# Optimization experiments

Measured on AMD Instinct MI355X. Metric: run time of the kernel, lower is better.

The kernel has to match this reference:

```python
import jax, jax.numpy as jnp
import numpy as np

B, S, DIM = 2, 2048, 2048
N_HEADS, N_KV = 16, 4
HEAD_DIM = DIM // N_HEADS
THETA = 10000.0


def _rope_tables(seq, half, theta):
    inv_freq = 1.0 / (theta ** (jnp.arange(0, half, dtype=jnp.float32) / half))
    t = jnp.arange(seq, dtype=jnp.float32)
    freqs = jnp.outer(t, inv_freq)  # (seq, half)
    return jnp.cos(freqs), jnp.sin(freqs)


def setup_inputs() -> dict:
    key = jax.random.key(0)
    ks = jax.random.split(key, 6)
    cos, sin = _rope_tables(S, HEAD_DIM // 2, THETA)
    scale_in = 1.0 / np.sqrt(DIM)
    return {
        "x": jax.random.normal(ks[0], (B, S, DIM), dtype=jnp.float32),
        "cos": cos,
        "sin": sin,
        "attn_mask": jax.random.randint(ks[1], (B, 1, 1, S), 0, 2) > 0,
        "Wq": jax.random.normal(ks[2], (N_HEADS * HEAD_DIM, DIM), dtype=jnp.float32) * scale_in,
        "Wk": jax.random.normal(ks[3], (N_KV * HEAD_DIM, DIM), dtype=jnp.float32) * scale_in,
        "Wv": jax.random.normal(ks[4], (N_KV * HEAD_DIM, DIM), dtype=jnp.float32) * scale_in,
        "Wo": jax.random.normal(ks[5], (DIM, N_HEADS * HEAD_DIM), dtype=jnp.float32) * scale_in,
    }


def _apply_rope(x, cos, sin):
    # x: (B, H, S, D); cos/sin: (S, D//2)
    D = x.shape[-1]
    x1, x2 = x[..., : D // 2], x[..., D // 2:]
    c = cos[None, None, : x.shape[2]]
    s = sin[None, None, : x.shape[2]]
    return jnp.concatenate([x1 * c - x2 * s, x1 * s + x2 * c], axis=-1)


def reference(x, cos, sin, attn_mask, Wq, Wk, Wv, Wo):
    b, s, _ = x.shape
    d = 2 * cos.shape[1]
    h = Wq.shape[0] // d
    kvh = Wk.shape[0] // d
    g = h // kvh  # query heads per KV head

    q = (x @ Wq.T).reshape(b, s, h, d).transpose(0, 2, 1, 3)     # (B,H,S,D)
    k = (x @ Wk.T).reshape(b, s, kvh, d).transpose(0, 2, 1, 3)   # (B,KV,S,D)
    v = (x @ Wv.T).reshape(b, s, kvh, d).transpose(0, 2, 1, 3)

    q = _apply_rope(q, cos, sin)
    k = _apply_rope(k, cos, sin)

    # Grouped attention without materializing repeated KV.
    qg = q.reshape(b, kvh, g, s, d)
    scores = jnp.einsum("bkgsd,bktd->bkgst", qg, k) / jnp.sqrt(jnp.asarray(d, q.dtype))
    mask = attn_mask[:, :, None]  # (B,1,1,1,S) broadcast over (B,KV,G,S,T)
    scores = jnp.where(mask, -jnp.inf, scores)
    attn = jax.nn.softmax(scores, axis=-1)
    out = jnp.einsum("bkgst,bktd->bkgsd", attn, v)
    out = out.reshape(b, h, s, d).transpose(0, 2, 1, 3).reshape(b, s, h * d)
    return out @ Wo.T
```

## Files before the change

kernel.cpp:

```cpp
#include <hip/hip_runtime.h>

typedef __attribute__((ext_vector_type(8))) short s16x8;
typedef __attribute__((ext_vector_type(4))) float f32x4;

#define B_    2
#define S_    2048
#define DIM_  2048
#define H_    16
#define KVH_  4
#define HD_   128
#define NQKV  3072

static __device__ __forceinline__ unsigned short f2bf(float f) {
  unsigned int u = __float_as_uint(f);
  u += 0x7fff + ((u >> 16) & 1);
  return (unsigned short)(u >> 16);
}
static __device__ __forceinline__ float bf2f(unsigned short h) {
  return __uint_as_float(((unsigned int)h) << 16);
}

__global__ __launch_bounds__(256) void cast_f32_bf16(const float* __restrict__ src,
                                                     unsigned short* __restrict__ dst, int n) {
  int i = (blockIdx.x * 256 + threadIdx.x) * 8;
  if (i >= n) return;
  float4 a = *(const float4*)(src + i);
  float4 b = *(const float4*)(src + i + 4);
  uint4 o;
  o.x = (unsigned)f2bf(a.x) | ((unsigned)f2bf(a.y) << 16);
  o.y = (unsigned)f2bf(a.z) | ((unsigned)f2bf(a.w) << 16);
  o.z = (unsigned)f2bf(b.x) | ((unsigned)f2bf(b.y) << 16);
  o.w = (unsigned)f2bf(b.z) | ((unsigned)f2bf(b.w) << 16);
  *(uint4*)(dst + i) = o;
}

template <bool BF16OUT>
__global__ __launch_bounds__(256) void gemm_bt(const unsigned short* __restrict__ A,
                                               const unsigned short* __restrict__ Bw,
                                               void* __restrict__ Cp, int N, int K) {
  __shared__ __align__(16) unsigned short As[128 * 32];
  __shared__ __align__(16) unsigned short Bs[128 * 32];
  const int tid = threadIdx.x;
  const int n0 = blockIdx.x * 128, m0 = blockIdx.y * 128;
  const int w = tid >> 6, l = tid & 63;
  const int wr = w >> 1, wc = w & 1;
  const int lo = l & 15, hi = l >> 4;
  f32x4 acc[4][4] = {};
  const int KT = K >> 5;
  for (int kt = 0; kt < KT; ++kt) {
    const int k0 = kt << 5;
    __syncthreads();
#pragma unroll
    for (int c = 0; c < 2; ++c) {
      int idx = tid + c * 256;
      int row = idx >> 2, ko = (idx & 3) << 3;
      __builtin_amdgcn_global_load_lds(
          (__attribute__((address_space(1))) void*)(A + (size_t)(m0 + row) * K + k0 + ko),
          (__attribute__((address_space(3))) void*)(As + idx * 8), 16, 0, 0);
      __builtin_amdgcn_global_load_lds(
          (__attribute__((address_space(1))) void*)(Bw + (size_t)(n0 + row) * K + k0 + ko),
          (__attribute__((address_space(3))) void*)(Bs + idx * 8), 16, 0, 0);
    }
    asm volatile("s_waitcnt vmcnt(0)" ::: "memory");
    __syncthreads();
    s16x8 af[4], bfr[4];
#pragma unroll
    for (int mi = 0; mi < 4; ++mi)
      af[mi] = *(const s16x8*)(As + (wr * 64 + mi * 16 + lo) * 32 + hi * 8);
#pragma unroll
    for (int ni = 0; ni < 4; ++ni)
      bfr[ni] = *(const s16x8*)(Bs + (wc * 64 + ni * 16 + lo) * 32 + hi * 8);
#pragma unroll
    for (int mi = 0; mi < 4; ++mi)
#pragma unroll
      for (int ni = 0; ni < 4; ++ni)
        acc[mi][ni] = __builtin_amdgcn_mfma_f32_16x16x32_bf16(af[mi], bfr[ni], acc[mi][ni], 0, 0, 0);
  }
#pragma unroll
  for (int mi = 0; mi < 4; ++mi) {
#pragma unroll
    for (int ni = 0; ni < 4; ++ni) {
      int col = n0 + wc * 64 + ni * 16 + lo;
      int rowb = m0 + wr * 64 + mi * 16 + hi * 4;
#pragma unroll
      for (int r = 0; r < 4; ++r) {
        float v = acc[mi][ni][r];
        if (BF16OUT)
          ((unsigned short*)Cp)[(size_t)(rowb + r) * N + col] = f2bf(v);
        else
          ((float*)Cp)[(size_t)(rowb + r) * N + col] = v;
      }
    }
  }
}

__global__ __launch_bounds__(256) void rope_kernel(const unsigned short* __restrict__ QKV,
                                                   const float* __restrict__ ctab,
                                                   const float* __restrict__ stab,
                                                   unsigned short* __restrict__ dst,
                                                   int nheads, int coloff, float scale) {
  int gid = blockIdx.x * 256 + threadIdx.x;
  int i = gid & 63;
  int rest = gid >> 6;
  int h = rest % nheads;
  int s = (rest / nheads) & (S_ - 1);
  int b = rest / (nheads * S_);
  const unsigned short* row = QKV + (size_t)(b * S_ + s) * NQKV + coloff + h * HD_;
  float x1 = bf2f(row[i]), x2 = bf2f(row[i + 64]);
  float c = ctab[s * 64 + i], sn = stab[s * 64 + i];
  unsigned short* drow = dst + ((size_t)(b * nheads + h) * S_ + s) * HD_;
  drow[i] = f2bf((x1 * c - x2 * sn) * scale);
  drow[i + 64] = f2bf((x1 * sn + x2 * c) * scale);
}

__global__ __launch_bounds__(256) void vtrans_kernel(const unsigned short* __restrict__ QKV,
                                                     unsigned short* __restrict__ Vt) {
  int s0 = blockIdx.x * 64;
  int d0 = blockIdx.y * 64;
  int bk = blockIdx.z;
  int b = bk >> 2, kvh = bk & 3;
  __shared__ __align__(16) unsigned short tile[64][72];
  int tid = threadIdx.x;
  for (int e = tid; e < 512; e += 256) {
    int r = e >> 3, c = (e & 7) << 3;
    const unsigned short* src =
        QKV + (size_t)(b * S_ + s0 + r) * NQKV + 2560 + kvh * HD_ + d0 + c;
    *(uint4*)(&tile[r][c]) = *(const uint4*)src;
  }
  __syncthreads();
  for (int e = tid; e < 512; e += 256) {
    int d = e >> 3, sc = (e & 7) << 3;
    unsigned int wv[4];
#pragma unroll
    for (int j = 0; j < 4; ++j)
      wv[j] = (unsigned)tile[sc + 2 * j][d] | ((unsigned)tile[sc + 2 * j + 1][d] << 16);
    uint4 o = {wv[0], wv[1], wv[2], wv[3]};
    unsigned short* dstp = Vt + ((size_t)bk * HD_ + d0 + d) * S_ + s0 + sc;
    *(uint4*)dstp = o;
  }
}

__global__ __launch_bounds__(512) void attn_kernel(const unsigned short* __restrict__ Qt,
                                                   const unsigned short* __restrict__ Kt,
                                                   const unsigned short* __restrict__ Vt,
                                                   const int* __restrict__ mask,
                                                   unsigned short* __restrict__ Out) {
  const int qt = blockIdx.x, h = blockIdx.y, b = blockIdx.z;
  const int kvh = h >> 2;
  const int tid = threadIdx.x, w = tid >> 6, l = tid & 63;
  const int lo = l & 15, hi = l >> 4;
  const int q0 = qt * 128 + w * 16;
  const unsigned short* Qb = Qt + ((size_t)(b * H_ + h) * S_ + q0) * HD_;
  const unsigned short* Kb = Kt + (size_t)(b * KVH_ + kvh) * S_ * HD_;
  const unsigned short* Vb = Vt + (size_t)(b * KVH_ + kvh) * HD_ * S_;
  const int* mb = mask + b * S_;

  __shared__ __align__(16) unsigned short Ks[64 * 128];
  __shared__ __align__(16) unsigned short Vs[128 * 64];
  __shared__ float bias[S_];
  __shared__ __align__(16) unsigned short P_lds[8][16 * 72];
  unsigned short* Pw = &P_lds[w][0];

  for (int i = tid; i < S_; i += 512) bias[i] = mb[i] ? -1e30f : 0.0f;

  s16x8 qf[4];
#pragma unroll
  for (int c = 0; c < 4; ++c)
    qf[c] = *(const s16x8*)(Qb + lo * HD_ + c * 32 + hi * 8);
  f32x4 o[8] = {};
  float mrow[4], lrow[4];
#pragma unroll
  for (int r = 0; r < 4; ++r) { mrow[r] = -1e30f; lrow[r] = 0.f; }

  for (int t0 = 0; t0 < S_; t0 += 64) {
    __syncthreads();
#pragma unroll
    for (int c = 0; c < 2; ++c) {
      int l4 = tid + c * 512;
      int r = l4 >> 4, ch = l4 & 15;
      int chg = (ch & 8) | ((ch ^ r) & 7);
      __builtin_amdgcn_global_load_lds(
          (__attribute__((address_space(1))) void*)(Kb + (size_t)(t0 + r) * HD_ + chg * 8),
          (__attribute__((address_space(3))) void*)(Ks + l4 * 8), 16, 0, 0);
    }
#pragma unroll
    for (int c = 0; c < 2; ++c) {
      int l4 = tid + c * 512;
      int d = l4 >> 3, ch = l4 & 7;
      int chg = (ch ^ d) & 7;
      __builtin_amdgcn_global_load_lds(
          (__attribute__((address_space(1))) void*)(Vb + (size_t)d * S_ + t0 + chg * 8),
          (__attribute__((address_space(3))) void*)(Vs + l4 * 8), 16, 0, 0);
    }
    asm volatile("s_waitcnt vmcnt(0)" ::: "memory");
    __syncthreads();

    f32x4 s[4];
#pragma unroll
    for (int sf = 0; sf < 4; ++sf) {
      f32x4 sv = {};
      int row = sf * 16 + lo;
#pragma unroll
      for (int c = 0; c < 4; ++c) {
        int ch = c * 4 + hi;
        int chs = (ch & 8) | ((ch ^ lo) & 7);
        s16x8 kf = *(const s16x8*)(Ks + row * 128 + chs * 8);
        sv = __builtin_amdgcn_mfma_f32_16x16x32_bf16(qf[c], kf, sv, 0, 0, 0);
      }
      float bv = bias[t0 + row];
#pragma unroll
      for (int r = 0; r < 4; ++r) sv[r] += bv;
      s[sf] = sv;
    }
    float tm[4];
#pragma unroll
    for (int r = 0; r < 4; ++r)
      tm[r] = fmaxf(fmaxf(s[0][r], s[1][r]), fmaxf(s[2][r], s[3][r]));
#pragma unroll
    for (int d = 1; d < 16; d <<= 1)
#pragma unroll
      for (int r = 0; r < 4; ++r) tm[r] = fmaxf(tm[r], __shfl_xor(tm[r], d));
    float sc_[4];
#pragma unroll
    for (int r = 0; r < 4; ++r) {
      float mnew = fmaxf(mrow[r], tm[r]);
      sc_[r] = __expf(mrow[r] - mnew);
      mrow[r] = mnew;
    }
#pragma unroll
    for (int df = 0; df < 8; ++df)
#pragma unroll
      for (int r = 0; r < 4; ++r) o[df][r] *= sc_[r];
    float ts[4] = {0.f, 0.f, 0.f, 0.f};
#pragma unroll
    for (int sf = 0; sf < 4; ++sf)
#pragma unroll
      for (int r = 0; r < 4; ++r) {
        float p = __expf(s[sf][r] - mrow[r]);
        ts[r] += p;
        Pw[(hi * 4 + r) * 72 + sf * 16 + lo] = f2bf(p);
      }
#pragma unroll
    for (int d = 1; d < 16; d <<= 1)
#pragma unroll
      for (int r = 0; r < 4; ++r) ts[r] += __shfl_xor(ts[r], d);
#pragma unroll
    for (int r = 0; r < 4; ++r) lrow[r] = lrow[r] * sc_[r] + ts[r];
    s16x8 pa[2];
#pragma unroll
    for (int kk = 0; kk < 2; ++kk)
      pa[kk] = *(const s16x8*)(Pw + lo * 72 + kk * 32 + hi * 8);
#pragma unroll
    for (int df = 0; df < 8; ++df) {
      int d = df * 16 + lo;
#pragma unroll
      for (int kk = 0; kk < 2; ++kk) {
        int ch = kk * 4 + hi;
        int chs = (ch ^ lo) & 7;
        s16x8 vf = *(const s16x8*)(Vs + d * 64 + chs * 8);
        o[df] = __builtin_amdgcn_mfma_f32_16x16x32_bf16(pa[kk], vf, o[df], 0, 0, 0);
      }
    }
  }
  float inv[4];
#pragma unroll
  for (int r = 0; r < 4; ++r) inv[r] = 1.0f / lrow[r];
#pragma unroll
  for (int df = 0; df < 8; ++df)
#pragma unroll
    for (int r = 0; r < 4; ++r)
      Out[(size_t)(b * S_ + q0 + hi * 4 + r) * DIM_ + h * HD_ + df * 16 + lo] =
          f2bf(o[df][r] * inv[r]);
}

extern "C" void kernel_launch(void* const* d_in, const int* in_sizes, int n_in,
                              void* d_out, int out_size, void* d_ws, size_t ws_size,
                              hipStream_t stream) {
  (void)in_sizes; (void)n_in; (void)out_size; (void)ws_size;
  const float* x    = (const float*)d_in[0];
  const float* ctab = (const float*)d_in[1];
  const float* stab = (const float*)d_in[2];
  const int*   mask = (const int*)d_in[3];
  const float* Wq   = (const float*)d_in[4];
  const float* Wk   = (const float*)d_in[5];
  const float* Wv   = (const float*)d_in[6];
  const float* Wo   = (const float*)d_in[7];

  unsigned short* x_bf = (unsigned short*)d_ws;
  unsigned short* Wqkv = x_bf + 8388608;
  unsigned short* Wob  = Wqkv + 6291456;
  unsigned short* QKV  = Wob + 4194304;
  unsigned short* Qt   = QKV + 12582912;
  unsigned short* Kt   = Qt + 8388608;
  unsigned short* Vt   = Kt + 2097152;

  cast_f32_bf16<<<4096, 256, 0, stream>>>(x, x_bf, 8388608);
  cast_f32_bf16<<<2048, 256, 0, stream>>>(Wq, Wqkv, 4194304);
  cast_f32_bf16<<<512, 256, 0, stream>>>(Wk, Wqkv + 4194304, 1048576);
  cast_f32_bf16<<<512, 256, 0, stream>>>(Wv, Wqkv + 5242880, 1048576);
  cast_f32_bf16<<<2048, 256, 0, stream>>>(Wo, Wob, 4194304);

  gemm_bt<true><<<dim3(24, 32), 256, 0, stream>>>(x_bf, Wqkv, QKV, NQKV, DIM_);

  rope_kernel<<<16384, 256, 0, stream>>>(QKV, ctab, stab, Qt, H_, 0, 0.08838834764831845f);
  rope_kernel<<<4096, 256, 0, stream>>>(QKV, ctab, stab, Kt, KVH_, DIM_, 1.0f);
  vtrans_kernel<<<dim3(32, 2, 8), 256, 0, stream>>>(QKV, Vt);

  attn_kernel<<<dim3(16, 16, 2), 512, 0, stream>>>(Qt, Kt, Vt, mask, x_bf);

  gemm_bt<false><<<dim3(16, 32), 256, 0, stream>>>(x_bf, Wob, d_out, DIM_, DIM_);
}
```

Baseline: 407.0 us.

## Fuse casts, swizzle block order, prefetch KV tiles and use exp2 lazy rescale

Merges the five cast launches into one kernel. Remaps block indices in the GEMM and attention kernels so neighbouring blocks share operands in cache. The attention loop now prefetches the next K/V tile into registers while it computes on the current one, reads the mask directly instead of staging a bias array in LDS, folds log2(e) into the Q scale so it can use exp2, and skips rescaling the running max unless the max grows by more than 8. Adds launch bounds for occupancy. The lazy rescale trades some numerical headroom for fewer multiplies, and the register prefetch adds register pressure and two barriers per iteration.

```diff
diff --git a/kernel.cpp b/kernel.cpp
--- a/kernel.cpp
+++ b/kernel.cpp
@@ -19,19 +19,40 @@
 static __device__ __forceinline__ float bf2f(unsigned short h) {
   return __uint_as_float(((unsigned int)h) << 16);
 }
-
-__global__ __launch_bounds__(256) void cast_f32_bf16(const float* __restrict__ src,
-                                                     unsigned short* __restrict__ dst, int n) {
-  int i = (blockIdx.x * 256 + threadIdx.x) * 8;
-  if (i >= n) return;
-  float4 a = *(const float4*)(src + i);
-  float4 b = *(const float4*)(src + i + 4);
+static __device__ __forceinline__ float fexp2(float x) {
+#if __has_builtin(__builtin_amdgcn_exp2f)
+  return __builtin_amdgcn_exp2f(x);
+#else
+  return exp2f(x);
+#endif
+}
+
+__global__ __launch_bounds__(256) void cast_all(const float* __restrict__ x,
+                                                const float* __restrict__ wq,
+                                                const float* __restrict__ wk,
+                                                const float* __restrict__ wv,
+                                                const float* __restrict__ wo,
+                                                unsigned short* __restrict__ xb,
+                                                unsigned short* __restrict__ wqkv,
+                                                unsigned short* __restrict__ wob) {
+  int blk = blockIdx.x;
+  const float* s;
+  unsigned short* d;
+  int rel;
+  if (blk < 4096)      { s = x;  d = xb;             rel = blk; }
+  else if (blk < 6144) { s = wq; d = wqkv;           rel = blk - 4096; }
+  else if (blk < 6656) { s = wk; d = wqkv + 4194304; rel = blk - 6144; }
+  else if (blk < 7168) { s = wv; d = wqkv + 5242880; rel = blk - 6656; }
+  else                 { s = wo; d = wob;            rel = blk - 7168; }
+  int i = (rel * 256 + threadIdx.x) * 8;
+  float4 a = *(const float4*)(s + i);
+  float4 b = *(const float4*)(s + i + 4);
   uint4 o;
   o.x = (unsigned)f2bf(a.x) | ((unsigned)f2bf(a.y) << 16);
   o.y = (unsigned)f2bf(a.z) | ((unsigned)f2bf(a.w) << 16);
   o.z = (unsigned)f2bf(b.x) | ((unsigned)f2bf(b.y) << 16);
   o.w = (unsigned)f2bf(b.z) | ((unsigned)f2bf(b.w) << 16);
-  *(uint4*)(dst + i) = o;
+  *(uint4*)(d + i) = o;
 }
 
 template <bool BF16OUT>
@@ -41,7 +62,11 @@
   __shared__ __align__(16) unsigned short As[128 * 32];
   __shared__ __align__(16) unsigned short Bs[128 * 32];
   const int tid = threadIdx.x;
-  const int n0 = blockIdx.x * 128, m0 = blockIdx.y * 128;
+  const int gx = gridDim.x;
+  const int lin = blockIdx.y * gx + blockIdx.x;
+  const int cpx = (gx * gridDim.y) >> 3;
+  const int nlin = (lin & 7) * cpx + (lin >> 3);
+  const int n0 = (nlin % gx) * 128, m0 = (nlin / gx) * 128;
   const int w = tid >> 6, l = tid & 63;
   const int wr = w >> 1, wc = w & 1;
   const int lo = l & 15, hi = l >> 4;
@@ -140,12 +165,14 @@
   }
 }
 
-__global__ __launch_bounds__(512) void attn_kernel(const unsigned short* __restrict__ Qt,
-                                                   const unsigned short* __restrict__ Kt,
-                                                   const unsigned short* __restrict__ Vt,
-                                                   const int* __restrict__ mask,
-                                                   unsigned short* __restrict__ Out) {
-  const int qt = blockIdx.x, h = blockIdx.y, b = blockIdx.z;
+__global__ __launch_bounds__(512, 4) void attn_kernel(const unsigned short* __restrict__ Qt,
+                                                      const unsigned short* __restrict__ Kt,
+                                                      const unsigned short* __restrict__ Vt,
+                                                      const int* __restrict__ mask,
+                                                      unsigned short* __restrict__ Out) {
+  const int lin = (blockIdx.z * gridDim.y + blockIdx.y) * gridDim.x + blockIdx.x;
+  const int nlin = (lin & 7) * 64 + (lin >> 3);
+  const int qt = nlin & 15, h = (nlin >> 4) & 15, b = nlin >> 8;
   const int kvh = h >> 2;
   const int tid = threadIdx.x, w = tid >> 6, l = tid & 63;
   const int lo = l & 15, hi = l >> 4;
@@ -157,43 +184,55 @@
 
   __shared__ __align__(16) unsigned short Ks[64 * 128];
   __shared__ __align__(16) unsigned short Vs[128 * 64];
-  __shared__ float bias[S_];
   __shared__ __align__(16) unsigned short P_lds[8][16 * 72];
   unsigned short* Pw = &P_lds[w][0];
 
-  for (int i = tid; i < S_; i += 512) bias[i] = mb[i] ? -1e30f : 0.0f;
-
   s16x8 qf[4];
 #pragma unroll
   for (int c = 0; c < 4; ++c)
     qf[c] = *(const s16x8*)(Qb + lo * HD_ + c * 32 + hi * 8);
+
+  int kl4[2], kchg[2], vl4[2], vchg[2], kr[2], vd[2];
+#pragma unroll
+  for (int c = 0; c < 2; ++c) {
+    int l4 = tid + c * 512;
+    kl4[c] = l4; kr[c] = l4 >> 4;
+    int ch = l4 & 15;
+    kchg[c] = (ch & 8) | ((ch ^ kr[c]) & 7);
+    vl4[c] = l4; vd[c] = l4 >> 3;
+    vchg[c] = ((l4 & 7) ^ vd[c]) & 7;
+  }
+
+#pragma unroll
+  for (int c = 0; c < 2; ++c) {
+    __builtin_amdgcn_global_load_lds(
+        (__attribute__((address_space(1))) void*)(Kb + (size_t)kr[c] * HD_ + kchg[c] * 8),
+        (__attribute__((address_space(3))) void*)(Ks + kl4[c] * 8), 16, 0, 0);
+    __builtin_amdgcn_global_load_lds(
+        (__attribute__((address_space(1))) void*)(Vb + (size_t)vd[c] * S_ + vchg[c] * 8),
+        (__attribute__((address_space(3))) void*)(Vs + vl4[c] * 8), 16, 0, 0);
+  }
+  asm volatile("s_waitcnt vmcnt(0)" ::: "memory");
+  __syncthreads();
+
   f32x4 o[8] = {};
   float mrow[4], lrow[4];
 #pragma unroll
   for (int r = 0; r < 4; ++r) { mrow[r] = -1e30f; lrow[r] = 0.f; }
 
   for (int t0 = 0; t0 < S_; t0 += 64) {
-    __syncthreads();
-#pragma unroll
-    for (int c = 0; c < 2; ++c) {
-      int l4 = tid + c * 512;
-      int r = l4 >> 4, ch = l4 & 15;
-      int chg = (ch & 8) | ((ch ^ r) & 7);
-      __builtin_amdgcn_global_load_lds(
-          (__attribute__((address_space(1))) void*)(Kb + (size_t)(t0 + r) * HD_ + chg * 8),
-          (__attribute__((address_space(3))) void*)(Ks + l4 * 8), 16, 0, 0);
-    }
-#pragma unroll
-    for (int c = 0; c < 2; ++c) {
-      int l4 = tid + c * 512;
-      int d = l4 >> 3, ch = l4 & 7;
-      int chg = (ch ^ d) & 7;
-      __builtin_amdgcn_global_load_lds(
-          (__attribute__((address_space(1))) void*)(Vb + (size_t)d * S_ + t0 + chg * 8),
-          (__attribute__((address_space(3))) void*)(Vs + l4 * 8), 16, 0, 0);
-    }
-    asm volatile("s_waitcnt vmcnt(0)" ::: "memory");
-    __syncthreads();
+    const bool has_next = (t0 + 64 < S_);
+    uint4 kreg[2], vreg[2];
+    if (has_next) {
+#pragma unroll
+      for (int c = 0; c < 2; ++c) {
+        kreg[c] = *(const uint4*)(Kb + (size_t)(t0 + 64 + kr[c]) * HD_ + kchg[c] * 8);
+        vreg[c] = *(const uint4*)(Vb + (size_t)vd[c] * S_ + t0 + 64 + vchg[c] * 8);
+      }
+    }
+    int mv[4];
+#pragma unroll
+    for (int sf = 0; sf < 4; ++sf) mv[sf] = mb[t0 + sf * 16 + lo];
 
     f32x4 s[4];
 #pragma unroll
@@ -207,7 +246,7 @@
         s16x8 kf = *(const s16x8*)(Ks + row * 128 + chs * 8);
         sv = __builtin_amdgcn_mfma_f32_16x16x32_bf16(qf[c], kf, sv, 0, 0, 0);
       }
-      float bv = bias[t0 + row];
+      float bv = mv[sf] ? -1e30f : 0.0f;
 #pragma unroll
       for (int r = 0; r < 4; ++r) sv[r] += bv;
       s[sf] = sv;
@@ -220,23 +259,29 @@
     for (int d = 1; d < 16; d <<= 1)
 #pragma unroll
       for (int r = 0; r < 4; ++r) tm[r] = fmaxf(tm[r], __shfl_xor(tm[r], d));
-    float sc_[4];
-#pragma unroll
-    for (int r = 0; r < 4; ++r) {
-      float mnew = fmaxf(mrow[r], tm[r]);
-      sc_[r] = __expf(mrow[r] - mnew);
-      mrow[r] = mnew;
-    }
-#pragma unroll
-    for (int df = 0; df < 8; ++df)
-#pragma unroll
-      for (int r = 0; r < 4; ++r) o[df][r] *= sc_[r];
+    float dm = tm[0] - mrow[0];
+#pragma unroll
+    for (int r = 1; r < 4; ++r) dm = fmaxf(dm, tm[r] - mrow[r]);
+    if (!__all(dm <= 8.0f)) {
+      float sc_[4];
+#pragma unroll
+      for (int r = 0; r < 4; ++r) {
+        float mnew = fmaxf(mrow[r], tm[r]);
+        sc_[r] = fexp2(mrow[r] - mnew);
+        mrow[r] = mnew;
+        lrow[r] *= sc_[r];
+      }
+#pragma unroll
+      for (int df = 0; df < 8; ++df)
+#pragma unroll
+        for (int r = 0; r < 4; ++r) o[df][r] *= sc_[r];
+    }
     float ts[4] = {0.f, 0.f, 0.f, 0.f};
 #pragma unroll
     for (int sf = 0; sf < 4; ++sf)
 #pragma unroll
       for (int r = 0; r < 4; ++r) {
-        float p = __expf(s[sf][r] - mrow[r]);
+        float p = fexp2(s[sf][r] - mrow[r]);
         ts[r] += p;
         Pw[(hi * 4 + r) * 72 + sf * 16 + lo] = f2bf(p);
       }
@@ -245,7 +290,7 @@
 #pragma unroll
       for (int r = 0; r < 4; ++r) ts[r] += __shfl_xor(ts[r], d);
 #pragma unroll
-    for (int r = 0; r < 4; ++r) lrow[r] = lrow[r] * sc_[r] + ts[r];
+    for (int r = 0; r < 4; ++r) lrow[r] += ts[r];
     s16x8 pa[2];
 #pragma unroll
     for (int kk = 0; kk < 2; ++kk)
@@ -261,6 +306,15 @@
         o[df] = __builtin_amdgcn_mfma_f32_16x16x32_bf16(pa[kk], vf, o[df], 0, 0, 0);
       }
     }
+    __syncthreads();
+    if (has_next) {
+#pragma unroll
+      for (int c = 0; c < 2; ++c) {
+        *(uint4*)(Ks + kl4[c] * 8) = kreg[c];
+        *(uint4*)(Vs + vl4[c] * 8) = vreg[c];
+      }
+    }
+    __syncthreads();
   }
   float inv[4];
 #pragma unroll
@@ -294,15 +348,12 @@
   unsigned short* Kt   = Qt + 8388608;
   unsigned short* Vt   = Kt + 2097152;
 
-  cast_f32_bf16<<<4096, 256, 0, stream>>>(x, x_bf, 8388608);
-  cast_f32_bf16<<<2048, 256, 0, stream>>>(Wq, Wqkv, 4194304);
-  cast_f32_bf16<<<512, 256, 0, stream>>>(Wk, Wqkv + 4194304, 1048576);
-  cast_f32_bf16<<<512, 256, 0, stream>>>(Wv, Wqkv + 5242880, 1048576);
-  cast_f32_bf16<<<2048, 256, 0, stream>>>(Wo, Wob, 4194304);
+  cast_all<<<9216, 256, 0, stream>>>(x, Wq, Wk, Wv, Wo, x_bf, Wqkv, Wob);
 
   gemm_bt<true><<<dim3(24, 32), 256, 0, stream>>>(x_bf, Wqkv, QKV, NQKV, DIM_);
 
-  rope_kernel<<<16384, 256, 0, stream>>>(QKV, ctab, stab, Qt, H_, 0, 0.08838834764831845f);
+  rope_kernel<<<16384, 256, 0, stream>>>(QKV, ctab, stab, Qt, H_, 0,
+                                         0.08838834764831845f * 1.4426950408889634f);
   rope_kernel<<<4096, 256, 0, stream>>>(QKV, ctab, stab, Kt, KVH_, DIM_, 1.0f);
   vtrans_kernel<<<dim3(32, 2, 8), 256, 0, stream>>>(QKV, Vt);
 
```

Measured after the change: 447.7 us. 10.0% more time.
